# Kernel tuning notes

Measured on AMD Instinct MI355X. Metric: run time of the kernel, lower is better.

## Reference

```python
import jax, jax.numpy as jnp
import numpy as np
import math

B, S, D, H, DH, R = 2, 2048, 1024, 16, 64, 8
EPS = 1e-5


def setup_inputs() -> dict:
    key = jax.random.key(0)
    ks = jax.random.split(key, 8)
    hidden_states = jax.random.normal(ks[0], (B, S, D), jnp.float32)
    # causal boolean mask (batch, seq, seq); every row has >=1 valid entry
    causal = jnp.tril(jnp.ones((S, S), dtype=bool))
    attention_mask = jnp.broadcast_to(causal, (B, S, S))
    # lora: (n_layers=1, 4, batch, hidden, rank); [0]=qA,[1]=kA,[2]=qB,[3]=kB
    lora = jax.random.normal(ks[1], (1, 4, B, D, R), jnp.float32) * 0.02
    ln_w = jnp.ones((D,), jnp.float32)
    Wq = jax.random.normal(ks[2], (D, D), jnp.float32) * 0.02
    Wk = jax.random.normal(ks[3], (D, D), jnp.float32) * 0.02
    Wv = jax.random.normal(ks[4], (D, D), jnp.float32) * 0.02
    Wo = jax.random.normal(ks[5], (D, D), jnp.float32) * 0.02
    return dict(hidden_states=hidden_states, attention_mask=attention_mask,
                lora=lora, ln_w=ln_w, Wq=Wq, Wk=Wk, Wv=Wv, Wo=Wo)


def _rms_ln(x, w):
    # model_center LayerNorm with bias=False == RMS layernorm
    var = jnp.mean(x * x, axis=-1, keepdims=True)
    return x * jax.lax.rsqrt(var + EPS) * w


def _lora_delta(h, A, Bm):
    # h: (b,s,D), A: (b,D,R), Bm: (b,R,D);  h + (h@A)@Bm * 2
    z = jnp.einsum('bsd,bdr->bsr', h, A)
    return h + jnp.einsum('bsr,brd->bsd', z, Bm) * 2


def reference(hidden_states, attention_mask, lora, ln_w, Wq, Wk, Wv, Wo):
    b, s, _ = hidden_states.shape
    x = _rms_ln(hidden_states, ln_w)
    h_q = x @ Wq.T
    h_k = x @ Wk.T
    h_v = x @ Wv.T
    layer = lora[0]  # (4, b, D, R)
    h_q = _lora_delta(h_q, layer[0], jnp.swapaxes(layer[2], 1, 2))
    h_k = _lora_delta(h_k, layer[1], jnp.swapaxes(layer[3], 1, 2))
    q = h_q.reshape(b, s, H, DH)
    k = h_k.reshape(b, s, H, DH)
    v = h_v.reshape(b, s, H, DH)
    score = jnp.einsum('bqhd,bkhd->bhqk', q, k) / math.sqrt(DH)
    m = attention_mask[:, None, :, :]  # (b,1,s,s)
    score = jnp.where(m, score, -jnp.inf)
    p = jax.nn.softmax(score, axis=-1)
    p = jnp.where(m, p, jnp.float32(0))
    out = jnp.einsum('bhqk,bkhd->bqhd', p, v).reshape(b, s, H * DH)
    out = out @ Wo.T
    return hidden_states + out
```

## Files before the change

kernel.cpp:

```cpp
#include <hip/hip_runtime.h>

typedef __bf16 bf16;
typedef __bf16 bf16x4 __attribute__((ext_vector_type(4)));
typedef __bf16 bf16x8 __attribute__((ext_vector_type(8)));
typedef float f32x4 __attribute__((ext_vector_type(4)));

#define DM 1024
#define NROW 4096
#define SEQ 2048
#define HDIM 64
#define NEGBIG -30000.0f

#define SWB(base, row, bcol) \
  ((char*)(base) + (row) * 128 + ((bcol) ^ (((row) & 7) << 4)))

__device__ __forceinline__ void async16(const bf16* g, bf16* l) {
  __builtin_amdgcn_global_load_lds(
      (const __attribute__((address_space(1))) unsigned int*)g,
      (__attribute__((address_space(3))) unsigned int*)l, 16, 0, 0);
}

template <bool F32OUT>
__device__ __forceinline__ void gemm128(const bf16* __restrict__ A,
                                        const bf16* __restrict__ Bw,
                                        bf16* __restrict__ Cb,
                                        float* __restrict__ Cf,
                                        const float* __restrict__ resid,
                                        int m0, int n0) {
  __shared__ __align__(16) bf16 sA[3][128 * 32];
  __shared__ __align__(16) bf16 sB[3][128 * 32];
  const int t = threadIdx.x;
  const int lane = t & 63;
  const int w = t >> 6;
  const int wm = (w & 1) * 64;
  const int wn = (w >> 1) * 64;
  const int lr = lane & 15;
  const int kg = lane >> 4;

  f32x4 acc[4][4];
#pragma unroll
  for (int i = 0; i < 4; i++)
#pragma unroll
    for (int j = 0; j < 4; j++)
#pragma unroll
      for (int r = 0; r < 4; r++) acc[i][j][r] = 0.0f;

  const int srow = t >> 2;
  const int scol = (t & 3) * 8;
  const bf16* gA = A + (size_t)(m0 + srow) * DM + scol;
  const bf16* gB = Bw + (size_t)(n0 + srow) * DM + scol;

#define GSTAGE(k0_, buf_)                                   \
  {                                                         \
    async16(gA + (k0_), &sA[buf_][t * 8]);                  \
    async16(gA + (k0_) + 64 * DM, &sA[buf_][t * 8 + 2048]); \
    async16(gB + (k0_), &sB[buf_][t * 8]);                  \
    async16(gB + (k0_) + 64 * DM, &sB[buf_][t * 8 + 2048]); \
  }

  GSTAGE(0, 0);
  GSTAGE(32, 1);

  int cur = 0;
  for (int k0 = 0; k0 < DM; k0 += 32) {
    const int n2 = (cur == 0) ? 2 : cur - 1;
    if (k0 + 64 < DM) {
      GSTAGE(k0 + 64, n2);
      asm volatile("s_waitcnt vmcnt(8)" ::: "memory");
    } else if (k0 + 32 < DM) {
      asm volatile("s_waitcnt vmcnt(4)" ::: "memory");
    } else {
      asm volatile("s_waitcnt vmcnt(0)" ::: "memory");
    }
    __builtin_amdgcn_s_barrier();

    bf16x8 av[4], bv[4];
#pragma unroll
    for (int mi = 0; mi < 4; mi++)
      av[mi] = *(const bf16x8*)&sA[cur][(wm + mi * 16 + lr) * 32 + kg * 8];
#pragma unroll
    for (int nj = 0; nj < 4; nj++)
      bv[nj] = *(const bf16x8*)&sB[cur][(wn + nj * 16 + lr) * 32 + kg * 8];
    __builtin_amdgcn_s_setprio(1);
#pragma unroll
    for (int mi = 0; mi < 4; mi++)
#pragma unroll
      for (int nj = 0; nj < 4; nj++)
        acc[mi][nj] = __builtin_amdgcn_mfma_f32_16x16x32_bf16(av[mi], bv[nj],
                                                              acc[mi][nj], 0, 0, 0);
    __builtin_amdgcn_s_setprio(0);
    __builtin_amdgcn_s_barrier();
    cur = (cur == 2) ? 0 : cur + 1;
  }
#undef GSTAGE

#pragma unroll
  for (int mi = 0; mi < 4; mi++) {
#pragma unroll
    for (int r = 0; r < 4; r++) {
      const int grow = m0 + wm + mi * 16 + kg * 4 + r;
      const size_t base = (size_t)grow * DM + n0 + wn + lr;
#pragma unroll
      for (int nj = 0; nj < 4; nj++) {
        float v = acc[mi][nj][r];
        if (F32OUT) {
          Cf[base + nj * 16] = v + resid[base + nj * 16];
        } else {
          Cb[base + nj * 16] = (bf16)v;
        }
      }
    }
  }
}

__global__ __launch_bounds__(256) void k_pre(const float* __restrict__ hin,
                                             const float* __restrict__ wln,
                                             const float* __restrict__ Wq,
                                             const float* __restrict__ Wk,
                                             const float* __restrict__ Wv,
                                             const float* __restrict__ Wo,
                                             bf16* __restrict__ xo,
                                             bf16* __restrict__ wcast) {
  __shared__ float red[4];
  const int t = threadIdx.x;
  const int bb = blockIdx.x;
  if (bb < NROW) {
    const int row = bb;
    const float4 h4 = ((const float4*)(hin + (size_t)row * DM))[t];
    float ss = h4.x * h4.x + h4.y * h4.y + h4.z * h4.z + h4.w * h4.w;
#pragma unroll
    for (int off = 1; off < 64; off <<= 1) ss += __shfl_xor(ss, off, 64);
    if ((t & 63) == 0) red[t >> 6] = ss;
    __syncthreads();
    ss = red[0] + red[1] + red[2] + red[3];
    const float inv = rsqrtf(ss * (1.0f / DM) + 1e-5f);
    const float4 w4 = ((const float4*)wln)[t];
    bf16x4 o;
    o[0] = (bf16)(h4.x * inv * w4.x);
    o[1] = (bf16)(h4.y * inv * w4.y);
    o[2] = (bf16)(h4.z * inv * w4.z);
    o[3] = (bf16)(h4.w * inv * w4.w);
    *(bf16x4*)&xo[(size_t)row * DM + t * 4] = o;
  } else {
    const int i = (bb - NROW) * 256 + t;
    const int mat = i >> 18;
    const int off = i & 262143;
    const float* s = (mat == 0) ? Wq : (mat == 1) ? Wk : (mat == 2) ? Wv : Wo;
    const float4 v = ((const float4*)s)[off];
    bf16x4 o;
    o[0] = (bf16)v.x; o[1] = (bf16)v.y; o[2] = (bf16)v.z; o[3] = (bf16)v.w;
    ((bf16x4*)wcast)[i] = o;
  }
}

__global__ __launch_bounds__(256) void k_qkv(const bf16* __restrict__ x,
                                             const bf16* __restrict__ Wq,
                                             const bf16* __restrict__ Wk,
                                             const bf16* __restrict__ Wv,
                                             bf16* __restrict__ hq,
                                             bf16* __restrict__ hk,
                                             bf16* __restrict__ hv) {
  const int nb = blockIdx.y;
  const int wsel = nb >> 3;
  const int n0 = (nb & 7) * 128;
  const bf16* Bw = (wsel == 0) ? Wq : (wsel == 1) ? Wk : Wv;
  bf16* C = (wsel == 0) ? hq : (wsel == 1) ? hk : hv;
  gemm128<false>(x, Bw, C, nullptr, nullptr, blockIdx.x * 128, n0);
}

__global__ __launch_bounds__(256) void k_oproj(const bf16* __restrict__ ctx,
                                               const bf16* __restrict__ Wo,
                                               const float* __restrict__ resid,
                                               float* __restrict__ out) {
  gemm128<true>(ctx, Wo, nullptr, out, resid, blockIdx.x * 128, blockIdx.y * 128);
}

__global__ __launch_bounds__(256) void k_mid(const bf16* __restrict__ hv,
                                             bf16* __restrict__ hvT,
                                             bf16* __restrict__ hq,
                                             bf16* __restrict__ hk,
                                             const float* __restrict__ lora) {
  __shared__ __align__(16) char smem[18432];
  const int t = threadIdx.x;
  const int bb = blockIdx.x;
  const int lane = t & 63;
  const int w = t >> 6;
  const int lr = lane & 15;
  const int kg = lane >> 4;

  if (bb < 1024) {
    bf16* sT = (bf16*)smem;
    const int s0 = (bb & 31) * 64;
    const int c0 = ((bb >> 5) & 15) * 64;
    const int b = bb >> 9;
    const int r = t >> 2;
    const int cc = (t & 3) * 16;
    const bf16* g = hv + ((size_t)(b * SEQ + s0 + r)) * DM + c0 + cc;
    const bf16x8 a0 = *(const bf16x8*)g;
    const bf16x8 a1 = *(const bf16x8*)(g + 8);
    *(bf16x8*)SWB(sT, r, cc * 2) = a0;
    *(bf16x8*)SWB(sT, r, cc * 2 + 16) = a1;
    __syncthreads();
    bf16x8 o0, o1;
#pragma unroll
    for (int j = 0; j < 8; j++) {
      o0[j] = *(const bf16*)SWB(sT, cc + j, r * 2);
      o1[j] = *(const bf16*)SWB(sT, cc + 8 + j, r * 2);
    }
    bf16* o = hvT + ((size_t)(b * DM + c0 + r)) * SEQ + s0 + cc;
    *(bf16x8*)o = o0;
    *(bf16x8*)(o + 8) = o1;
  } else {
    bf16* At = (bf16*)smem;
    float* Zp = (float*)(smem + 16384);
    const int lid = bb - 1024;
    const int row0 = (lid & 127) * 32;
    const int which = lid >> 7;
    const int b = row0 >> 11;
    bf16* H = (which == 0 ? hq : hk) + (size_t)row0 * DM;
    const float* Am = lora + (size_t)(which == 0 ? 0 : 1) * 16384 + (size_t)b * 8192;
    const float* Bm = lora + (size_t)(which == 0 ? 2 : 3) * 16384 + (size_t)b * 8192;

    const int d0 = lane * 16;
    float4 Bv[32];
    {
      const float4* bp = (const float4*)(Bm + (size_t)d0 * 8);
#pragma unroll
      for (int i = 0; i < 32; i++) Bv[i] = bp[i];
    }

    {
      const float4* ap = (const float4*)(Am + (size_t)t * 32);
#pragma unroll
      for (int i = 0; i < 8; i++) {
        const float4 v = ap[i];
        const int idx = t * 32 + i * 4;
        At[(idx & 7) * 1024 + (idx >> 3)]             = (bf16)v.x;
        At[((idx + 1) & 7) * 1024 + ((idx + 1) >> 3)] = (bf16)v.y;
        At[((idx + 2) & 7) * 1024 + ((idx + 2) >> 3)] = (bf16)v.z;
        At[((idx + 3) & 7) * 1024 + ((idx + 3) >> 3)] = (bf16)v.w;
      }
    }
    __syncthreads();

    const int tile = w & 1;
    const int khalf = w >> 1;
    {
      f32x4 zacc;
#pragma unroll
      for (int r = 0; r < 4; r++) zacc[r] = 0.f;
      const bf16* gH = H + (size_t)(tile * 16 + lr) * DM + khalf * 512 + kg * 8;
      const bf16* lA = &At[(lr & 7) * 1024 + khalf * 512 + kg * 8];
#pragma unroll
      for (int i = 0; i < 16; i++) {
        const bf16x8 ah = *(const bf16x8*)(gH + i * 32);
        const bf16x8 ba = *(const bf16x8*)(lA + i * 32);
        zacc = __builtin_amdgcn_mfma_f32_16x16x32_bf16(ah, ba, zacc, 0, 0, 0);
      }
      if (lr < 8) {
#pragma unroll
        for (int r = 0; r < 4; r++)
          Zp[(khalf * 32 + tile * 16 + kg * 4 + r) * 8 + lr] = zacc[r];
      }
    }
    __syncthreads();

#pragma unroll
    for (int rr = 0; rr < 8; rr++) {
      const int row = w * 8 + rr;
      const float4 z0 = *(const float4*)&Zp[(row) * 8 + 0];
      const float4 z1 = *(const float4*)&Zp[(row) * 8 + 4];
      const float4 y0 = *(const float4*)&Zp[(32 + row) * 8 + 0];
      const float4 y1 = *(const float4*)&Zp[(32 + row) * 8 + 4];
      const float za = z0.x + y0.x, zb = z0.y + y0.y, zc = z0.z + y0.z, zd = z0.w + y0.w;
      const float ze = z1.x + y1.x, zf = z1.y + y1.y, zg = z1.z + y1.z, zh = z1.w + y1.w;
      bf16* hp = H + (size_t)row * DM + d0;
      const bf16x8 h0 = *(const bf16x8*)hp;
      const bf16x8 h1 = *(const bf16x8*)(hp + 8);
      bf16x8 o0, o1;
#pragma unroll
      for (int j = 0; j < 16; j++) {
        const float4 b0 = Bv[2 * j];
        const float4 b1 = Bv[2 * j + 1];
        const float delta = za * b0.x + zb * b0.y + zc * b0.z + zd * b0.w +
                            ze * b1.x + zf * b1.y + zg * b1.z + zh * b1.w;
        const float hj = (j < 8) ? (float)h0[j] : (float)h1[j - 8];
        const bf16 ov = (bf16)(hj + 2.0f * delta);
        if (j < 8) o0[j] = ov; else o1[j - 8] = ov;
      }
      *(bf16x8*)hp = o0;
      *(bf16x8*)(hp + 8) = o1;
    }
  }
}

__global__ __launch_bounds__(256, 4) void k_attn(const bf16* __restrict__ hq,
                                                 const bf16* __restrict__ hk,
                                                 const bf16* __restrict__ hvT,
                                                 bf16* __restrict__ ctx) {
  const int n = blockIdx.x;
  const int slab = n & 31;
  const int hh = slab & 15;
  const int b = slab >> 4;
  const int xx = n >> 5;
  const int s = xx >> 3;
  const int v = xx & 7;
  const int qt = (s == 0) ? 4 * v : (s == 1) ? 31 - 4 * v
               : (s == 2) ? 4 * v + 2 : 29 - 4 * v;
  const int qbase = qt * 64;

  const int t = threadIdx.x;
  const int lane = t & 63;
  const int w = t >> 6;
  const int lr = lane & 15;
  const int kg = lane >> 4;

  __shared__ __align__(16) bf16 sQ[64 * 64];
  __shared__ __align__(16) bf16 sK[64 * 64];
  __shared__ __align__(16) bf16 sVt[64 * 64];
  __shared__ __align__(16) bf16 sP[64 * 64];

  const size_t rowbase = (size_t)b * SEQ;
  const int hoff = hh * HDIM;
  const float sscale = 0.18033688011112042f;

  const int r4 = t >> 2;
  const int ce = (t & 3) * 16;
  const int cb = (t & 3) * 32;

  {
    const bf16* g = hq + (rowbase + qbase + r4) * DM + hoff + ce;
    bf16x8 q0 = *(const bf16x8*)g;
    bf16x8 q1 = *(const bf16x8*)(g + 8);
    bf16x8 o0, o1;
#pragma unroll
    for (int j = 0; j < 8; j++) {
      o0[j] = (bf16)((float)q0[j] * sscale);
      o1[j] = (bf16)((float)q1[j] * sscale);
    }
    *(bf16x8*)SWB(sQ, r4, cb) = o0;
    *(bf16x8*)SWB(sQ, r4, cb + 16) = o1;
  }

  const bf16* gK = hk + (rowbase + r4) * DM + hoff + ce;
  const bf16* gV = hvT + ((size_t)slab * HDIM + r4) * SEQ + ce;
  bf16x8 kr0 = *(const bf16x8*)gK;
  bf16x8 kr1 = *(const bf16x8*)(gK + 8);
  bf16x8 vr0 = *(const bf16x8*)gV;
  bf16x8 vr1 = *(const bf16x8*)(gV + 8);

  float m_l = NEGBIG, l_l = 0.f;
  f32x4 oacc[4];
#pragma unroll
  for (int nj = 0; nj < 4; nj++)
#pragma unroll
    for (int r = 0; r < 4; r++) oacc[nj][r] = 0.f;

  __syncthreads();

  for (int kt = 0; kt <= qt; kt++) {
    *(bf16x8*)SWB(sK, r4, cb) = kr0;
    *(bf16x8*)SWB(sK, r4, cb + 16) = kr1;
    *(bf16x8*)SWB(sVt, r4, cb) = vr0;
    *(bf16x8*)SWB(sVt, r4, cb + 16) = vr1;
    __syncthreads();

    if (kt < qt) {
      const bf16* gK2 = gK + (size_t)(kt + 1) * 64 * DM;
      const bf16* gV2 = gV + (kt + 1) * 64;
      kr0 = *(const bf16x8*)gK2;
      kr1 = *(const bf16x8*)(gK2 + 8);
      vr0 = *(const bf16x8*)gV2;
      vr1 = *(const bf16x8*)(gV2 + 8);
    }

    f32x4 sc[4];
#pragma unroll
    for (int nj = 0; nj < 4; nj++)
#pragma unroll
      for (int r = 0; r < 4; r++) sc[nj][r] = 0.f;
    __builtin_amdgcn_s_setprio(1);
#pragma unroll
    for (int ks = 0; ks < 2; ks++) {
      const bf16x8 bq = *(const bf16x8*)SWB(sQ, w * 16 + lr, ks * 64 + kg * 16);
#pragma unroll
      for (int nj = 0; nj < 4; nj++) {
        const bf16x8 ak = *(const bf16x8*)SWB(sK, nj * 16 + lr, ks * 64 + kg * 16);
        sc[nj] = __builtin_amdgcn_mfma_f32_16x16x32_bf16(ak, bq, sc[nj], 0, 0, 0);
      }
    }
    __builtin_amdgcn_s_setprio(0);

    if (kt == qt) {
      const int ql = w * 16 + lr;
#pragma unroll
      for (int nj = 0; nj < 4; nj++)
#pragma unroll
        for (int r = 0; r < 4; r++) {
          const int kl = nj * 16 + kg * 4 + r;
          sc[nj][r] = (kl <= ql) ? sc[nj][r] : NEGBIG;
        }
    }

    float rm = sc[0][0];
#pragma unroll
    for (int nj = 0; nj < 4; nj++)
#pragma unroll
      for (int r = 0; r < 4; r++) rm = fmaxf(rm, sc[nj][r]);
    rm = fmaxf(rm, __shfl_xor(rm, 16, 64));
    rm = fmaxf(rm, __shfl_xor(rm, 32, 64));

    const bool skip = __all(rm - m_l <= 8.0f);
    if (!skip) {
      const float mnew = fmaxf(m_l, rm);
      const float alpha = __builtin_amdgcn_exp2f(m_l - mnew);
      l_l *= alpha;
      m_l = mnew;
#pragma unroll
      for (int r = 0; r < 4; r++) {
        const float ar = __shfl(alpha, (lane & 48) | (kg * 4 + r), 64);
#pragma unroll
        for (int nj = 0; nj < 4; nj++) oacc[nj][r] *= ar;
      }
    }

    float rs = 0.f;
#pragma unroll
    for (int nj = 0; nj < 4; nj++)
#pragma unroll
      for (int r = 0; r < 4; r++) {
        const float p = __builtin_amdgcn_exp2f(sc[nj][r] - m_l);
        sc[nj][r] = p;
        rs += p;
      }
    rs += __shfl_xor(rs, 16, 64);
    rs += __shfl_xor(rs, 32, 64);
    l_l += rs;

#pragma unroll
    for (int nj = 0; nj < 4; nj++) {
      bf16x4 p4;
#pragma unroll
      for (int r = 0; r < 4; r++) p4[r] = (bf16)sc[nj][r];
      *(bf16x4*)SWB(sP, w * 16 + lr, nj * 32 + kg * 8) = p4;
    }

    __builtin_amdgcn_s_setprio(1);
#pragma unroll
    for (int ks = 0; ks < 2; ks++) {
      const bf16x8 ap = *(const bf16x8*)SWB(sP, w * 16 + lr, ks * 64 + kg * 16);
#pragma unroll
      for (int nj = 0; nj < 4; nj++) {
        const bf16x8 bv = *(const bf16x8*)SWB(sVt, nj * 16 + lr, ks * 64 + kg * 16);
        oacc[nj] = __builtin_amdgcn_mfma_f32_16x16x32_bf16(ap, bv, oacc[nj], 0, 0, 0);
      }
    }
    __builtin_amdgcn_s_setprio(0);
    __syncthreads();
  }

#pragma unroll
  for (int r = 0; r < 4; r++) {
    const float lrow = __shfl(l_l, (lane & 48) | (kg * 4 + r), 64);
    const float invl = 1.0f / lrow;
    const int qr = qbase + w * 16 + kg * 4 + r;
    const size_t base = (rowbase + qr) * DM + hoff + lr;
#pragma unroll
    for (int nj = 0; nj < 4; nj++)
      ctx[base + nj * 16] = (bf16)(oacc[nj][r] * invl);
  }
}

extern "C" void kernel_launch(void* const* d_in, const int* in_sizes, int n_in,
                              void* d_out, int out_size, void* d_ws, size_t ws_size,
                              hipStream_t stream) {
  const float* hidden = (const float*)d_in[0];
  const float* lora = (const float*)d_in[2];
  const float* wln  = (const float*)d_in[3];
  const float* Wq   = (const float*)d_in[4];
  const float* Wk   = (const float*)d_in[5];
  const float* Wv   = (const float*)d_in[6];
  const float* Wo   = (const float*)d_in[7];
  float* out = (float*)d_out;

  const size_t BUF = (size_t)NROW * DM;
  if (ws_size < 4 * BUF * sizeof(bf16)) return;
  bf16* ws = (bf16*)d_ws;
  bf16* hq  = ws;
  bf16* hk  = ws + 1 * BUF;
  bf16* hv  = ws + 2 * BUF;
  bf16* ctx = ws + 3 * BUF;

  bf16* dob = (bf16*)d_out;
  bf16* x   = dob;
  bf16* wqb = dob + BUF;
  bf16* wkb = dob + BUF + DM * DM;
  bf16* wvb = dob + BUF + 2 * DM * DM;
  bf16* wob = dob + BUF + 3 * DM * DM;
  bf16* hvT = dob;

  k_pre<<<dim3(2 * NROW), dim3(256), 0, stream>>>(hidden, wln, Wq, Wk, Wv, Wo, x, wqb);
  k_qkv<<<dim3(32, 24), dim3(256), 0, stream>>>(x, wqb, wkb, wvb, hq, hk, hv);
  k_mid<<<dim3(1280), dim3(256), 0, stream>>>(hv, hvT, hq, hk, lora);
  k_attn<<<dim3(1024), dim3(256), 0, stream>>>(hq, hk, hvT, ctx);
  k_oproj<<<dim3(32, 8), dim3(256), 0, stream>>>(ctx, wob, hidden, out);
}
```

Baseline: 220.3 us.

## Fuse V transpose into QKV GEMM epilogue and widen o-proj blocks to 8 waves

The V projection GEMM now writes its output directly in the transposed (b, d, s) layout that attention consumes. This removes the separate transpose stage in k_mid, which shrinks to only the LoRA update blocks. The output projection is rewritten as a 512-thread kernel with 8 waves per 128x128 tile, each wave covering 64x32, to raise latency hiding. The transposed epilogue uses narrower, strided 8-byte stores, which may coalesce worse.

```diff
diff --git a/kernel.cpp b/kernel.cpp
--- a/kernel.cpp
+++ b/kernel.cpp
@@ -20,7 +20,7 @@
       (__attribute__((address_space(3))) unsigned int*)l, 16, 0, 0);
 }
 
-template <bool F32OUT>
+template <int MODE>
 __device__ __forceinline__ void gemm128(const bf16* __restrict__ A,
                                         const bf16* __restrict__ Bw,
                                         bf16* __restrict__ Cb,
@@ -94,6 +94,24 @@
   }
 #undef GSTAGE
 
+  if (MODE == 2) {
+    const int bb2 = m0 >> 11;
+    const int sbase = (m0 & 2047) + wm + kg * 4;
+#pragma unroll
+    for (int mi = 0; mi < 4; mi++) {
+#pragma unroll
+      for (int nj = 0; nj < 4; nj++) {
+        bf16x4 o;
+#pragma unroll
+        for (int r = 0; r < 4; r++) o[r] = (bf16)acc[mi][nj][r];
+        const int col = n0 + wn + nj * 16 + lr;
+        bf16* dst = Cb + ((size_t)(bb2 * 1024 + col)) * SEQ + sbase + mi * 16;
+        *(bf16x4*)dst = o;
+      }
+    }
+    return;
+  }
+
 #pragma unroll
   for (int mi = 0; mi < 4; mi++) {
 #pragma unroll
@@ -103,7 +121,7 @@
 #pragma unroll
       for (int nj = 0; nj < 4; nj++) {
         float v = acc[mi][nj][r];
-        if (F32OUT) {
+        if (MODE == 1) {
           Cf[base + nj * 16] = v + resid[base + nj * 16];
         } else {
           Cb[base + nj * 16] = (bf16)v;
@@ -159,138 +177,192 @@
                                              const bf16* __restrict__ Wv,
                                              bf16* __restrict__ hq,
                                              bf16* __restrict__ hk,
-                                             bf16* __restrict__ hv) {
+                                             bf16* __restrict__ hvT) {
   const int nb = blockIdx.y;
   const int wsel = nb >> 3;
   const int n0 = (nb & 7) * 128;
-  const bf16* Bw = (wsel == 0) ? Wq : (wsel == 1) ? Wk : Wv;
-  bf16* C = (wsel == 0) ? hq : (wsel == 1) ? hk : hv;
-  gemm128<false>(x, Bw, C, nullptr, nullptr, blockIdx.x * 128, n0);
-}
-
-__global__ __launch_bounds__(256) void k_oproj(const bf16* __restrict__ ctx,
+  const int m0 = blockIdx.x * 128;
+  if (wsel == 2) {
+    gemm128<2>(x, Wv, hvT, nullptr, nullptr, m0, n0);
+  } else {
+    gemm128<0>(x, (wsel == 0) ? Wq : Wk, (wsel == 0) ? hq : hk,
+               nullptr, nullptr, m0, n0);
+  }
+}
+
+__global__ __launch_bounds__(512) void k_oproj(const bf16* __restrict__ ctx,
                                                const bf16* __restrict__ Wo,
                                                const float* __restrict__ resid,
                                                float* __restrict__ out) {
-  gemm128<true>(ctx, Wo, nullptr, out, resid, blockIdx.x * 128, blockIdx.y * 128);
-}
-
-__global__ __launch_bounds__(256) void k_mid(const bf16* __restrict__ hv,
-                                             bf16* __restrict__ hvT,
-                                             bf16* __restrict__ hq,
+  __shared__ __align__(16) bf16 sA[3][128 * 32];
+  __shared__ __align__(16) bf16 sB[3][128 * 32];
+  const int t = threadIdx.x;
+  const int lane = t & 63;
+  const int w = t >> 6;
+  const int wm = (w & 1) * 64;
+  const int wn = (w >> 1) * 32;
+  const int lr = lane & 15;
+  const int kg = lane >> 4;
+  const int m0 = blockIdx.x * 128;
+  const int n0 = blockIdx.y * 128;
+
+  f32x4 acc[4][2];
+#pragma unroll
+  for (int i = 0; i < 4; i++)
+#pragma unroll
+    for (int j = 0; j < 2; j++)
+#pragma unroll
+      for (int r = 0; r < 4; r++) acc[i][j][r] = 0.0f;
+
+  const int srow = t >> 2;
+  const int scol = (t & 3) * 8;
+  const bf16* gA = ctx + (size_t)(m0 + srow) * DM + scol;
+  const bf16* gB = Wo + (size_t)(n0 + srow) * DM + scol;
+
+#define GSTAGE8(k0_, buf_)                      \
+  {                                             \
+    async16(gA + (k0_), &sA[buf_][t * 8]);      \
+    async16(gB + (k0_), &sB[buf_][t * 8]);      \
+  }
+
+  GSTAGE8(0, 0);
+  GSTAGE8(32, 1);
+
+  int cur = 0;
+  for (int k0 = 0; k0 < DM; k0 += 32) {
+    const int n2 = (cur == 0) ? 2 : cur - 1;
+    if (k0 + 64 < DM) {
+      GSTAGE8(k0 + 64, n2);
+      asm volatile("s_waitcnt vmcnt(4)" ::: "memory");
+    } else if (k0 + 32 < DM) {
+      asm volatile("s_waitcnt vmcnt(2)" ::: "memory");
+    } else {
+      asm volatile("s_waitcnt vmcnt(0)" ::: "memory");
+    }
+    __builtin_amdgcn_s_barrier();
+
+    bf16x8 av[4], bv[2];
+#pragma unroll
+    for (int mi = 0; mi < 4; mi++)
+      av[mi] = *(const bf16x8*)&sA[cur][(wm + mi * 16 + lr) * 32 + kg * 8];
+#pragma unroll
+    for (int nj = 0; nj < 2; nj++)
+      bv[nj] = *(const bf16x8*)&sB[cur][(wn + nj * 16 + lr) * 32 + kg * 8];
+    __builtin_amdgcn_s_setprio(1);
+#pragma unroll
+    for (int mi = 0; mi < 4; mi++)
+#pragma unroll
+      for (int nj = 0; nj < 2; nj++)
+        acc[mi][nj] = __builtin_amdgcn_mfma_f32_16x16x32_bf16(av[mi], bv[nj],
+                                                              acc[mi][nj], 0, 0, 0);
+    __builtin_amdgcn_s_setprio(0);
+    __builtin_amdgcn_s_barrier();
+    cur = (cur == 2) ? 0 : cur + 1;
+  }
+#undef GSTAGE8
+
+#pragma unroll
+  for (int mi = 0; mi < 4; mi++) {
+#pragma unroll
+    for (int r = 0; r < 4; r++) {
+      const int grow = m0 + wm + mi * 16 + kg * 4 + r;
+      const size_t base = (size_t)grow * DM + n0 + wn + lr;
+#pragma unroll
+      for (int nj = 0; nj < 2; nj++)
+        out[base + nj * 16] = acc[mi][nj][r] + resid[base + nj * 16];
+    }
+  }
+}
+
+__global__ __launch_bounds__(256) void k_mid(bf16* __restrict__ hq,
                                              bf16* __restrict__ hk,
                                              const float* __restrict__ lora) {
   __shared__ __align__(16) char smem[18432];
   const int t = threadIdx.x;
-  const int bb = blockIdx.x;
+  const int lid = blockIdx.x;
   const int lane = t & 63;
   const int w = t >> 6;
   const int lr = lane & 15;
   const int kg = lane >> 4;
 
-  if (bb < 1024) {
-    bf16* sT = (bf16*)smem;
-    const int s0 = (bb & 31) * 64;
-    const int c0 = ((bb >> 5) & 15) * 64;
-    const int b = bb >> 9;
-    const int r = t >> 2;
-    const int cc = (t & 3) * 16;
-    const bf16* g = hv + ((size_t)(b * SEQ + s0 + r)) * DM + c0 + cc;
-    const bf16x8 a0 = *(const bf16x8*)g;
-    const bf16x8 a1 = *(const bf16x8*)(g + 8);
-    *(bf16x8*)SWB(sT, r, cc * 2) = a0;
-    *(bf16x8*)SWB(sT, r, cc * 2 + 16) = a1;
-    __syncthreads();
+  bf16* At = (bf16*)smem;
+  float* Zp = (float*)(smem + 16384);
+  const int row0 = (lid & 127) * 32;
+  const int which = lid >> 7;
+  const int b = row0 >> 11;
+  bf16* H = (which == 0 ? hq : hk) + (size_t)row0 * DM;
+  const float* Am = lora + (size_t)(which == 0 ? 0 : 1) * 16384 + (size_t)b * 8192;
+  const float* Bm = lora + (size_t)(which == 0 ? 2 : 3) * 16384 + (size_t)b * 8192;
+
+  const int d0 = lane * 16;
+  float4 Bv[32];
+  {
+    const float4* bp = (const float4*)(Bm + (size_t)d0 * 8);
+#pragma unroll
+    for (int i = 0; i < 32; i++) Bv[i] = bp[i];
+  }
+
+  {
+    const float4* ap = (const float4*)(Am + (size_t)t * 32);
+#pragma unroll
+    for (int i = 0; i < 8; i++) {
+      const float4 v = ap[i];
+      const int idx = t * 32 + i * 4;
+      At[(idx & 7) * 1024 + (idx >> 3)]             = (bf16)v.x;
+      At[((idx + 1) & 7) * 1024 + ((idx + 1) >> 3)] = (bf16)v.y;
+      At[((idx + 2) & 7) * 1024 + ((idx + 2) >> 3)] = (bf16)v.z;
+      At[((idx + 3) & 7) * 1024 + ((idx + 3) >> 3)] = (bf16)v.w;
+    }
+  }
+  __syncthreads();
+
+  const int tile = w & 1;
+  const int khalf = w >> 1;
+  {
+    f32x4 zacc;
+#pragma unroll
+    for (int r = 0; r < 4; r++) zacc[r] = 0.f;
+    const bf16* gH = H + (size_t)(tile * 16 + lr) * DM + khalf * 512 + kg * 8;
+    const bf16* lA = &At[(lr & 7) * 1024 + khalf * 512 + kg * 8];
+#pragma unroll
+    for (int i = 0; i < 16; i++) {
+      const bf16x8 ah = *(const bf16x8*)(gH + i * 32);
+      const bf16x8 ba = *(const bf16x8*)(lA + i * 32);
+      zacc = __builtin_amdgcn_mfma_f32_16x16x32_bf16(ah, ba, zacc, 0, 0, 0);
+    }
+    if (lr < 8) {
+#pragma unroll
+      for (int r = 0; r < 4; r++)
+        Zp[(khalf * 32 + tile * 16 + kg * 4 + r) * 8 + lr] = zacc[r];
+    }
+  }
+  __syncthreads();
+
+#pragma unroll
+  for (int rr = 0; rr < 8; rr++) {
+    const int row = w * 8 + rr;
+    const float4 z0 = *(const float4*)&Zp[(row) * 8 + 0];
+    const float4 z1 = *(const float4*)&Zp[(row) * 8 + 4];
+    const float4 y0 = *(const float4*)&Zp[(32 + row) * 8 + 0];
+    const float4 y1 = *(const float4*)&Zp[(32 + row) * 8 + 4];
+    const float za = z0.x + y0.x, zb = z0.y + y0.y, zc = z0.z + y0.z, zd = z0.w + y0.w;
+    const float ze = z1.x + y1.x, zf = z1.y + y1.y, zg = z1.z + y1.z, zh = z1.w + y1.w;
+    bf16* hp = H + (size_t)row * DM + d0;
+    const bf16x8 h0 = *(const bf16x8*)hp;
+    const bf16x8 h1 = *(const bf16x8*)(hp + 8);
     bf16x8 o0, o1;
 #pragma unroll
-    for (int j = 0; j < 8; j++) {
-      o0[j] = *(const bf16*)SWB(sT, cc + j, r * 2);
-      o1[j] = *(const bf16*)SWB(sT, cc + 8 + j, r * 2);
-    }
-    bf16* o = hvT + ((size_t)(b * DM + c0 + r)) * SEQ + s0 + cc;
-    *(bf16x8*)o = o0;
-    *(bf16x8*)(o + 8) = o1;
-  } else {
-    bf16* At = (bf16*)smem;
-    float* Zp = (float*)(smem + 16384);
-    const int lid = bb - 1024;
-    const int row0 = (lid & 127) * 32;
-    const int which = lid >> 7;
-    const int b = row0 >> 11;
-    bf16* H = (which == 0 ? hq : hk) + (size_t)row0 * DM;
-    const float* Am = lora + (size_t)(which == 0 ? 0 : 1) * 16384 + (size_t)b * 8192;
-    const float* Bm = lora + (size_t)(which == 0 ? 2 : 3) * 16384 + (size_t)b * 8192;
-
-    const int d0 = lane * 16;
-    float4 Bv[32];
-    {
-      const float4* bp = (const float4*)(Bm + (size_t)d0 * 8);
-#pragma unroll
-      for (int i = 0; i < 32; i++) Bv[i] = bp[i];
-    }
-
-    {
-      const float4* ap = (const float4*)(Am + (size_t)t * 32);
-#pragma unroll
-      for (int i = 0; i < 8; i++) {
-        const float4 v = ap[i];
-        const int idx = t * 32 + i * 4;
-        At[(idx & 7) * 1024 + (idx >> 3)]             = (bf16)v.x;
-        At[((idx + 1) & 7) * 1024 + ((idx + 1) >> 3)] = (bf16)v.y;
-        At[((idx + 2) & 7) * 1024 + ((idx + 2) >> 3)] = (bf16)v.z;
-        At[((idx + 3) & 7) * 1024 + ((idx + 3) >> 3)] = (bf16)v.w;
-      }
-    }
-    __syncthreads();
-
-    const int tile = w & 1;
-    const int khalf = w >> 1;
-    {
-      f32x4 zacc;
-#pragma unroll
-      for (int r = 0; r < 4; r++) zacc[r] = 0.f;
-      const bf16* gH = H + (size_t)(tile * 16 + lr) * DM + khalf * 512 + kg * 8;
-      const bf16* lA = &At[(lr & 7) * 1024 + khalf * 512 + kg * 8];
-#pragma unroll
-      for (int i = 0; i < 16; i++) {
-        const bf16x8 ah = *(const bf16x8*)(gH + i * 32);
-        const bf16x8 ba = *(const bf16x8*)(lA + i * 32);
-        zacc = __builtin_amdgcn_mfma_f32_16x16x32_bf16(ah, ba, zacc, 0, 0, 0);
-      }
-      if (lr < 8) {
-#pragma unroll
-        for (int r = 0; r < 4; r++)
-          Zp[(khalf * 32 + tile * 16 + kg * 4 + r) * 8 + lr] = zacc[r];
-      }
-    }
-    __syncthreads();
-
-#pragma unroll
-    for (int rr = 0; rr < 8; rr++) {
-      const int row = w * 8 + rr;
-      const float4 z0 = *(const float4*)&Zp[(row) * 8 + 0];
-      const float4 z1 = *(const float4*)&Zp[(row) * 8 + 4];
-      const float4 y0 = *(const float4*)&Zp[(32 + row) * 8 + 0];
-      const float4 y1 = *(const float4*)&Zp[(32 + row) * 8 + 4];
-      const float za = z0.x + y0.x, zb = z0.y + y0.y, zc = z0.z + y0.z, zd = z0.w + y0.w;
-      const float ze = z1.x + y1.x, zf = z1.y + y1.y, zg = z1.z + y1.z, zh = z1.w + y1.w;
-      bf16* hp = H + (size_t)row * DM + d0;
-      const bf16x8 h0 = *(const bf16x8*)hp;
-      const bf16x8 h1 = *(const bf16x8*)(hp + 8);
-      bf16x8 o0, o1;
-#pragma unroll
-      for (int j = 0; j < 16; j++) {
-        const float4 b0 = Bv[2 * j];
-        const float4 b1 = Bv[2 * j + 1];
-        const float delta = za * b0.x + zb * b0.y + zc * b0.z + zd * b0.w +
-                            ze * b1.x + zf * b1.y + zg * b1.z + zh * b1.w;
-        const float hj = (j < 8) ? (float)h0[j] : (float)h1[j - 8];
-        const bf16 ov = (bf16)(hj + 2.0f * delta);
-        if (j < 8) o0[j] = ov; else o1[j - 8] = ov;
-      }
-      *(bf16x8*)hp = o0;
-      *(bf16x8*)(hp + 8) = o1;
-    }
+    for (int j = 0; j < 16; j++) {
+      const float4 b0 = Bv[2 * j];
+      const float4 b1 = Bv[2 * j + 1];
+      const float delta = za * b0.x + zb * b0.y + zc * b0.z + zd * b0.w +
+                          ze * b1.x + zf * b1.y + zg * b1.z + zh * b1.w;
+      const float hj = (j < 8) ? (float)h0[j] : (float)h1[j - 8];
+      const bf16 ov = (bf16)(hj + 2.0f * delta);
+      if (j < 8) o0[j] = ov; else o1[j - 8] = ov;
+    }
+    *(bf16x8*)hp = o0;
+    *(bf16x8*)(hp + 8) = o1;
   }
 }
 
@@ -488,7 +560,7 @@
   bf16* ws = (bf16*)d_ws;
   bf16* hq  = ws;
   bf16* hk  = ws + 1 * BUF;
-  bf16* hv  = ws + 2 * BUF;
+  bf16* hvT = ws + 2 * BUF;
   bf16* ctx = ws + 3 * BUF;
 
   bf16* dob = (bf16*)d_out;
@@ -497,11 +569,10 @@
   bf16* wkb = dob + BUF + DM * DM;
   bf16* wvb = dob + BUF + 2 * DM * DM;
   bf16* wob = dob + BUF + 3 * DM * DM;
-  bf16* hvT = dob;
 
   k_pre<<<dim3(2 * NROW), dim3(256), 0, stream>>>(hidden, wln, Wq, Wk, Wv, Wo, x, wqb);
-  k_qkv<<<dim3(32, 24), dim3(256), 0, stream>>>(x, wqb, wkb, wvb, hq, hk, hv);
-  k_mid<<<dim3(1280), dim3(256), 0, stream>>>(hv, hvT, hq, hk, lora);
+  k_qkv<<<dim3(32, 24), dim3(256), 0, stream>>>(x, wqb, wkb, wvb, hq, hk, hvT);
+  k_mid<<<dim3(256), dim3(256), 0, stream>>>(hq, hk, lora);
   k_attn<<<dim3(1024), dim3(256), 0, stream>>>(hq, hk, hvT, ctx);
-  k_oproj<<<dim3(32, 8), dim3(256), 0, stream>>>(ctx, wob, hidden, out);
-}
+  k_oproj<<<dim3(32, 8), dim3(512), 0, stream>>>(ctx, wob, hidden, out);
+}
```

New measurement: 243.6 us. 1.11x slower.
